# Performance work log

Hardware: AMD Instinct MI355X
Metric: run time of the kernel (lower is better)

## Reference

```python
import jax, jax.numpy as jnp
import numpy as np

B, T, F, D, HD = 16, 512, 16, 256, 256


def _init(k, shape, fan_in):
    return (jax.random.uniform(k, shape, minval=-1.0, maxval=1.0) / np.sqrt(fan_in)).astype(jnp.float32)


def setup_inputs() -> dict:
    key = jax.random.key(0)
    ks = jax.random.split(key, 16)
    return {
        "x": jax.random.normal(ks[0], (B, T, F), dtype=jnp.float32),
        # per-variable encoder params, batched over F (Linear(1,D) + GRN(D,HD,D))
        "w1": _init(ks[1], (F, D), 1), "b1": _init(ks[2], (F, D), 1),
        "fc1_w": _init(ks[3], (F, D, HD), D), "fc1_b": _init(ks[4], (F, HD), D),
        "fc2_w": _init(ks[5], (F, HD, D), HD), "fc2_b": _init(ks[6], (F, D), HD),
        "glu_w": _init(ks[7], (F, D, 2 * D), D), "glu_b": _init(ks[8], (F, 2 * D), D),
        "ln_g": jnp.ones((F, D), jnp.float32), "ln_b": jnp.zeros((F, D), jnp.float32),
        # weight GRN(F, HD, F); skip is Identity since d_in == d_out
        "wg_fc1_w": _init(ks[9], (F, HD), F), "wg_fc1_b": _init(ks[10], (HD,), F),
        "wg_fc2_w": _init(ks[11], (HD, F), HD), "wg_fc2_b": _init(ks[12], (F,), HD),
        "wg_glu_w": _init(ks[13], (F, 2 * F), F), "wg_glu_b": _init(ks[14], (2 * F,), F),
        "wg_ln_g": jnp.ones((F,), jnp.float32), "wg_ln_b": jnp.zeros((F,), jnp.float32),
    }


def _layernorm(x, g, b, eps=1e-5):
    m = jnp.mean(x, axis=-1, keepdims=True)
    v = jnp.var(x, axis=-1, keepdims=True)
    return (x - m) * jax.lax.rsqrt(v + eps) * g + b


def reference(x, w1, b1, fc1_w, fc1_b, fc2_w, fc2_b, glu_w, glu_b, ln_g, ln_b,
              wg_fc1_w, wg_fc1_b, wg_fc2_w, wg_fc2_b, wg_glu_w, wg_glu_b,
              wg_ln_g, wg_ln_b):
    # --- per-variable towers, batched over F (dropout is identity at eval) ---
    h0 = jax.nn.relu(x[..., None] * w1 + b1)                       # [B,T,F,D]
    y = jax.nn.elu(jnp.einsum('btfd,fdh->btfh', h0, fc1_w) + fc1_b)
    y = jnp.einsum('btfh,fhd->btfd', y, fc2_w) + fc2_b
    g = jnp.einsum('btfd,fde->btfe', y, glu_w) + glu_b             # [B,T,F,2D]
    a, gate = jnp.split(g, 2, axis=-1)
    H = _layernorm(h0 + a * jax.nn.sigmoid(gate), ln_g, ln_b)      # [B,T,F,D]
    # --- variable-weight GRN (time_distributed=True) ---
    yw = jax.nn.elu(x @ wg_fc1_w + wg_fc1_b)
    yw = yw @ wg_fc2_w + wg_fc2_b
    gw = x @ jnp.zeros((F, 0), x.dtype) if False else yw @ wg_glu_w + wg_glu_b
    aw, gatew = jnp.split(gw, 2, axis=-1)
    w = _layernorm(x + aw * jax.nn.sigmoid(gatew), wg_ln_g, wg_ln_b)
    w = jax.nn.softmax(w, axis=-1)                                 # [B,T,F]
    z = jnp.einsum('btfd,btf->btd', H, w)                          # [B,T,D]
    return z, w
```

## Files before the change

### kernel.cpp

```cpp
#include <hip/hip_runtime.h>
#include <hip/hip_bf16.h>

#define NBT 8192
#define NF  16
#define ND  256
#define NH  256
#define N2D 512

typedef short bf16x8 __attribute__((ext_vector_type(8)));
typedef float f32x4 __attribute__((ext_vector_type(4)));
typedef unsigned short u16x8 __attribute__((ext_vector_type(8)));

__device__ __forceinline__ float bf2f(unsigned short u) {
  return __uint_as_float(((unsigned)u) << 16);
}
__device__ __forceinline__ unsigned short f2bf(float f) {
  unsigned u = __float_as_uint(f);
  return (unsigned short)((u + 0x7FFFu + ((u >> 16) & 1u)) >> 16);
}

#define GLOAD16(src, dst)                                                     \
  __builtin_amdgcn_global_load_lds(                                           \
      (const __attribute__((address_space(1))) unsigned int*)(src),           \
      (__attribute__((address_space(3))) unsigned int*)(dst), 16, 0, 0)

__global__ __launch_bounds__(256) void wgrn_kernel(
    const float* __restrict__ x, const float* __restrict__ fw1,
    const float* __restrict__ fb1, const float* __restrict__ fw2,
    const float* __restrict__ fb2, const float* __restrict__ gwt,
    const float* __restrict__ gbt, const float* __restrict__ lng,
    const float* __restrict__ lnb, float* __restrict__ wout) {
  __shared__ float w1t[256 * 16];
  __shared__ float w2s[256 * 16];
  const int tid = threadIdx.x;
  for (int i = tid; i < 4096; i += 256) {
    int ff = i >> 8, j = i & 255;
    w1t[j * 16 + ff] = fw1[i];
    w2s[i] = fw2[i];
  }
  __syncthreads();
  const int sub  = tid & 7;
  const int rowi = tid >> 3;
  const int bt   = blockIdx.x * 32 + rowi;
  float xr[16];
#pragma unroll
  for (int i = 0; i < 4; ++i)
    *(float4*)&xr[i * 4] = *(const float4*)(x + (size_t)bt * 16 + i * 4);
  float acc2[16];
#pragma unroll
  for (int q = 0; q < 16; ++q) acc2[q] = 0.f;
  for (int j = sub; j < 256; j += 8) {
    float h = fb1[j];
    const float* wr = &w1t[j * 16];
#pragma unroll
    for (int q = 0; q < 16; ++q) h = fmaf(xr[q], wr[q], h);
    h = h > 0.f ? h : expm1f(h);
    const float* w2r = &w2s[j * 16];
#pragma unroll
    for (int q = 0; q < 16; ++q) acc2[q] = fmaf(h, w2r[q], acc2[q]);
  }
#pragma unroll
  for (int off = 1; off < 8; off <<= 1) {
#pragma unroll
    for (int q = 0; q < 16; ++q) acc2[q] += __shfl_xor(acc2[q], off);
  }
#pragma unroll
  for (int q = 0; q < 16; ++q) acc2[q] += fb2[q];
  float gw[32];
#pragma unroll
  for (int k = 0; k < 32; ++k) {
    float s = gbt[k];
#pragma unroll
    for (int q = 0; q < 16; ++q) s = fmaf(acc2[q], gwt[q * 32 + k], s);
    gw[k] = s;
  }
  float v[16];
  float mean = 0.f;
#pragma unroll
  for (int q = 0; q < 16; ++q) {
    float sg = 1.f / (1.f + __expf(-gw[16 + q]));
    v[q] = fmaf(gw[q], sg, xr[q]);
    mean += v[q];
  }
  mean *= (1.f / 16.f);
  float var = 0.f;
#pragma unroll
  for (int q = 0; q < 16; ++q) { float d = v[q] - mean; var = fmaf(d, d, var); }
  var *= (1.f / 16.f);
  float rstd = rsqrtf(var + 1e-5f);
  float mx = -1e30f;
#pragma unroll
  for (int q = 0; q < 16; ++q) {
    v[q] = (v[q] - mean) * rstd * lng[q] + lnb[q];
    mx = fmaxf(mx, v[q]);
  }
  float se = 0.f;
#pragma unroll
  for (int q = 0; q < 16; ++q) { v[q] = __expf(v[q] - mx); se += v[q]; }
  float inv = 1.f / se;
  if (sub == 0) {
#pragma unroll
    for (int i = 0; i < 4; ++i) {
      float4 o = { v[i*4+0]*inv, v[i*4+1]*inv, v[i*4+2]*inv, v[i*4+3]*inv };
      *(float4*)(wout + (size_t)bt * 16 + i * 4) = o;
    }
  }
}

__global__ void transpose_all(const float* __restrict__ fc1_w,
                              const float* __restrict__ fc2_w,
                              const float* __restrict__ glu_w,
                              unsigned short* __restrict__ fc1t,
                              unsigned short* __restrict__ fc2t,
                              unsigned short* __restrict__ glut) {
  __shared__ float tile[32][33];
  const int which = blockIdx.z >> 4;
  const int f     = blockIdx.z & 15;
  const float* src;
  unsigned short* dst;
  int K, N, bx = blockIdx.x;
  if (which == 0)      { src = fc1_w; dst = fc1t; K = ND; N = NH; }
  else if (which == 1) { src = fc2_w; dst = fc2t; K = NH; N = ND; }
  else                 { src = glu_w; dst = glut; K = ND; N = N2D;
                         bx += (which == 3) ? 8 : 0; }
  if (bx * 32 >= N) return;
  const float* s = src + (size_t)f * K * N;
  unsigned short* d = dst + (size_t)f * K * N;
  const int k0 = blockIdx.y * 32, n0 = bx * 32;
  const int tx = threadIdx.x, ty = threadIdx.y;
#pragma unroll
  for (int i = 0; i < 32; i += 8)
    tile[ty + i][tx] = s[(size_t)(k0 + ty + i) * N + n0 + tx];
  __syncthreads();
#pragma unroll
  for (int i = 0; i < 32; i += 8)
    d[(size_t)(n0 + ty + i) * K + k0 + tx] = f2bf(tile[tx][ty + i]);
}

__global__ __launch_bounds__(512, 2) void g12_kernel(
    const float* __restrict__ x, const float* __restrict__ w1,
    const float* __restrict__ b1, const unsigned short* __restrict__ fc1t,
    const float* __restrict__ fc1_b, const unsigned short* __restrict__ fc2t,
    const float* __restrict__ fc2_b, unsigned short* __restrict__ y2) {
  __shared__ __align__(16) unsigned short hbuf[64 * 264];
  __shared__ __align__(16) unsigned short bstg[256 * 64];
  __shared__ float xw[64];
  const int tid = threadIdx.x, lane = tid & 63, wid = tid >> 6;
  const int rl = lane & 15, kc = lane >> 4;
  int hb = blockIdx.x + 128 * blockIdx.y;
  int L  = (hb & 7) * 256 + (hb >> 3);
  const int f = L >> 7, m0 = (L & 127) * 64;
  const unsigned short* B1 = fc1t + (size_t)f * NH * ND;
  const unsigned short* B2 = fc2t + (size_t)f * ND * NH;
  const float* w1f = w1 + f * ND;
  const float* b1f = b1 + f * ND;
  const int wn = wid * 32;

  if (tid < 64) xw[tid] = x[(size_t)(m0 + tid) * NF + f];
  __syncthreads();

#pragma unroll
  for (int i = 0; i < 4; ++i) {
    int j = tid + 512 * i;
    int row = j >> 5, c = (j & 31) * 8;
    float xv = xw[row];
    float4 wa = *(const float4*)(w1f + c);
    float4 wb = *(const float4*)(w1f + c + 4);
    float4 ba = *(const float4*)(b1f + c);
    float4 bb = *(const float4*)(b1f + c + 4);
    u16x8 o;
    o[0] = f2bf(fmaxf(fmaf(xv, wa.x, ba.x), 0.f));
    o[1] = f2bf(fmaxf(fmaf(xv, wa.y, ba.y), 0.f));
    o[2] = f2bf(fmaxf(fmaf(xv, wa.z, ba.z), 0.f));
    o[3] = f2bf(fmaxf(fmaf(xv, wa.w, ba.w), 0.f));
    o[4] = f2bf(fmaxf(fmaf(xv, wb.x, bb.x), 0.f));
    o[5] = f2bf(fmaxf(fmaf(xv, wb.y, bb.y), 0.f));
    o[6] = f2bf(fmaxf(fmaf(xv, wb.z, bb.z), 0.f));
    o[7] = f2bf(fmaxf(fmaf(xv, wb.w, bb.w), 0.f));
    *(u16x8*)(hbuf + row * 264 + c) = o;
  }
  __syncthreads();

  f32x4 acc[4][2];
#pragma unroll
  for (int m = 0; m < 4; ++m)
#pragma unroll
    for (int n = 0; n < 2; ++n) acc[m][n] = (f32x4){0.f, 0.f, 0.f, 0.f};

  for (int kt = 0; kt < ND; kt += 64) {
    if (kt) __syncthreads();
#pragma unroll
    for (int i = 0; i < 4; ++i) {
      int s = tid + 512 * i;
      int row = s >> 3, sl = s & 7;
      GLOAD16(B1 + (size_t)row * ND + kt + ((sl ^ (row & 7)) << 3),
              (char*)bstg + (wid * 64 + 512 * i) * 16);
    }
    __syncthreads();
#pragma unroll
    for (int kk = 0; kk < 2; ++kk) {
      int s = kk * 4 + kc;
      bf16x8 av[4], bv[2];
#pragma unroll
      for (int n = 0; n < 2; ++n) {
        int rr = wn + n * 16 + rl;
        int ps = s ^ (rr & 7);
        bv[n] = *(const bf16x8*)((const char*)bstg + rr * 128 + ps * 16);
      }
#pragma unroll
      for (int m = 0; m < 4; ++m)
        av[m] = *(const bf16x8*)(hbuf + (m * 16 + rl) * 264 + kt + s * 8);
#pragma unroll
      for (int m = 0; m < 4; ++m)
#pragma unroll
        for (int n = 0; n < 2; ++n)
          acc[m][n] = __builtin_amdgcn_mfma_f32_16x16x32_bf16(av[m], bv[n],
                                                              acc[m][n], 0, 0, 0);
    }
  }
  __syncthreads();

#pragma unroll
  for (int n = 0; n < 2; ++n) {
    int c = wn + n * 16 + rl;
    float bvv = fc1_b[f * NH + c];
#pragma unroll
    for (int m = 0; m < 4; ++m) {
#pragma unroll
      for (int j = 0; j < 4; ++j) {
        int r = m * 16 + kc * 4 + j;
        float v = acc[m][n][j] + bvv;
        v = v > 0.f ? v : expm1f(v);
        hbuf[r * 264 + c] = f2bf(v);
      }
    }
  }
  __syncthreads();

#pragma unroll
  for (int m = 0; m < 4; ++m)
#pragma unroll
    for (int n = 0; n < 2; ++n) acc[m][n] = (f32x4){0.f, 0.f, 0.f, 0.f};

  for (int kt = 0; kt < NH; kt += 64) {
    if (kt) __syncthreads();
#pragma unroll
    for (int i = 0; i < 4; ++i) {
      int s = tid + 512 * i;
      int row = s >> 3, sl = s & 7;
      GLOAD16(B2 + (size_t)row * NH + kt + ((sl ^ (row & 7)) << 3),
              (char*)bstg + (wid * 64 + 512 * i) * 16);
    }
    __syncthreads();
#pragma unroll
    for (int kk = 0; kk < 2; ++kk) {
      int s = kk * 4 + kc;
      bf16x8 av[4], bv[2];
#pragma unroll
      for (int n = 0; n < 2; ++n) {
        int rr = wn + n * 16 + rl;
        int ps = s ^ (rr & 7);
        bv[n] = *(const bf16x8*)((const char*)bstg + rr * 128 + ps * 16);
      }
#pragma unroll
      for (int m = 0; m < 4; ++m)
        av[m] = *(const bf16x8*)(hbuf + (m * 16 + rl) * 264 + kt + s * 8);
#pragma unroll
      for (int m = 0; m < 4; ++m)
#pragma unroll
        for (int n = 0; n < 2; ++n)
          acc[m][n] = __builtin_amdgcn_mfma_f32_16x16x32_bf16(av[m], bv[n],
                                                              acc[m][n], 0, 0, 0);
    }
  }
  __syncthreads();

#pragma unroll
  for (int n = 0; n < 2; ++n) {
    int c = wn + n * 16 + rl;
    float bvv = fc2_b[f * ND + c];
#pragma unroll
    for (int m = 0; m < 4; ++m) {
#pragma unroll
      for (int j = 0; j < 4; ++j) {
        int r = m * 16 + kc * 4 + j;
        hbuf[r * 264 + c] = f2bf(acc[m][n][j] + bvv);
      }
    }
  }
  __syncthreads();
#pragma unroll
  for (int v = 0; v < 4; ++v) {
    int job = tid + 512 * v;
    int row = job >> 5, ch = job & 31;
    u16x8 val = *(const u16x8*)(hbuf + row * 264 + ch * 8);
    *(u16x8*)(y2 + ((size_t)f * NBT + m0 + row) * ND + ch * 8) = val;
  }
}

__global__ __launch_bounds__(512, 4) void g3_kernel(
    const unsigned short* __restrict__ y2,
    const unsigned short* __restrict__ glut, const float* __restrict__ glu_b,
    const float* __restrict__ x, const float* __restrict__ w1,
    const float* __restrict__ b1, const float* __restrict__ ln_g,
    const float* __restrict__ ln_b, unsigned short* __restrict__ H) {
  __shared__ __align__(16) char arena[73728];
  __shared__ float xw[64];
  __shared__ float2 sums[8][64];
  __shared__ float2 sums2[64];
  unsigned short* abuf = (unsigned short*)arena;
  unsigned short* bbuf = (unsigned short*)(arena + 8192);
  unsigned short* vbuf = (unsigned short*)arena;

  const int tid = threadIdx.x, lane = tid & 63, wid = tid >> 6;
  const int rl = lane & 15, rq = lane >> 4;
  int hb = blockIdx.x + 128 * blockIdx.y;
  int L  = (hb & 7) * 256 + (hb >> 3);
  const int f = L >> 7, m0 = (L & 127) * 64;
  const unsigned short* Af = y2 + (size_t)f * NBT * ND;
  const unsigned short* Bf = glut + (size_t)f * ND * N2D;
  const float* w1f = w1 + f * ND;
  const float* b1f = b1 + f * ND;
  const int colb = wid * 32;
  if (tid < 64) xw[tid] = x[(size_t)(m0 + tid) * NF + f];

  f32x4 acc[4][4];
#pragma unroll
  for (int m = 0; m < 4; ++m)
#pragma unroll
    for (int n = 0; n < 4; ++n) acc[m][n] = (f32x4){0.f, 0.f, 0.f, 0.f};

  for (int kt = 0; kt < ND; kt += 64) {
    __syncthreads();
    {
      int s = tid;
      int row = s >> 3, sl = s & 7;
      const unsigned short* ga =
          Af + (size_t)(m0 + row) * ND + kt + ((sl ^ (row & 7)) << 3);
      GLOAD16(ga, (char*)abuf + (wid * 64) * 16);
    }
#pragma unroll
    for (int i = 0; i < 8; ++i) {
      int s = tid + 512 * i;
      int row = s >> 3, sl = s & 7;
      const unsigned short* gb =
          Bf + (size_t)row * ND + kt + ((sl ^ (row & 7)) << 3);
      GLOAD16(gb, (char*)bbuf + (wid * 64 + 512 * i) * 16);
    }
    __syncthreads();
#pragma unroll
    for (int kk = 0; kk < 2; ++kk) {
      bf16x8 av[4], bv[4];
      int s = kk * 4 + rq;
#pragma unroll
      for (int m = 0; m < 4; ++m) {
        int r = m * 16 + rl;
        int ps = s ^ (r & 7);
        av[m] = *(const bf16x8*)((const char*)abuf + r * 128 + ps * 16);
      }
#pragma unroll
      for (int n = 0; n < 4; ++n) {
        int rr = (n < 2) ? (colb + n * 16 + rl)
                         : (256 + colb + (n - 2) * 16 + rl);
        int ps = s ^ (rr & 7);
        bv[n] = *(const bf16x8*)((const char*)bbuf + rr * 128 + ps * 16);
      }
#pragma unroll
      for (int m = 0; m < 4; ++m)
#pragma unroll
        for (int n = 0; n < 4; ++n)
          acc[m][n] = __builtin_amdgcn_mfma_f32_16x16x32_bf16(av[m], bv[n],
                                                              acc[m][n], 0, 0, 0);
    }
  }

#pragma unroll
  for (int n = 0; n < 2; ++n) {
    int cA = colb + n * 16 + rl;
    float ab_ = glu_b[f * N2D + cA];
    float gb_ = glu_b[f * N2D + 256 + cA];
    float w1c = w1f[cA], b1c = b1f[cA];
#pragma unroll
    for (int m = 0; m < 4; ++m) {
#pragma unroll
      for (int j = 0; j < 4; ++j) {
        int r = m * 16 + rq * 4 + j;
        float a = acc[m][n][j] + ab_;
        float g = acc[m][n + 2][j] + gb_;
        float sg = 1.f / (1.f + __expf(-g));
        float h0 = fmaxf(fmaf(xw[r], w1c, b1c), 0.f);
        acc[m][n][j] = fmaf(a, sg, h0);
      }
    }
  }
#pragma unroll
  for (int m = 0; m < 4; ++m) {
#pragma unroll
    for (int j = 0; j < 4; ++j) {
      float s = acc[m][0][j] + acc[m][1][j];
      float q = fmaf(acc[m][0][j], acc[m][0][j],
                     acc[m][1][j] * acc[m][1][j]);
#pragma unroll
      for (int off = 1; off < 16; off <<= 1) {
        s += __shfl_xor(s, off);
        q += __shfl_xor(q, off);
      }
      if (rl == 0) sums[wid][m * 16 + rq * 4 + j] = make_float2(s, q);
    }
  }
  __syncthreads();
  if (tid < 64) {
    float tot = 0.f, tot2 = 0.f;
#pragma unroll
    for (int wv = 0; wv < 8; ++wv) {
      float2 p = sums[wv][tid];
      tot += p.x;
      tot2 += p.y;
    }
    float mean = tot * (1.f / 256.f);
    float var  = tot2 * (1.f / 256.f) - mean * mean;
    sums2[tid] = make_float2(mean, rsqrtf(var + 1e-5f));
  }
  __syncthreads();
#pragma unroll
  for (int n = 0; n < 2; ++n) {
    int cA = colb + n * 16 + rl;
    float lg = ln_g[f * ND + cA], lb = ln_b[f * ND + cA];
#pragma unroll
    for (int m = 0; m < 4; ++m) {
#pragma unroll
      for (int j = 0; j < 4; ++j) {
        int r = m * 16 + rq * 4 + j;
        float2 mr = sums2[r];
        vbuf[r * 264 + cA] = f2bf(fmaf((acc[m][n][j] - mr.x) * mr.y, lg, lb));
      }
    }
  }
  __syncthreads();
  {
    int row = tid >> 3, chunk = tid & 7;
    unsigned short* Hrow = H + ((size_t)f * NBT + m0 + row) * ND;
#pragma unroll
    for (int v = 0; v < 4; ++v) {
      u16x8 val = *(const u16x8*)(vbuf + row * 264 + chunk * 8 + v * 64);
      *(u16x8*)(Hrow + chunk * 8 + v * 64) = val;
    }
  }
}

__global__ __launch_bounds__(256) void combine_kernel(
    const unsigned short* __restrict__ H, const float* __restrict__ w,
    float* __restrict__ z) {
  int idx = blockIdx.x * 256 + threadIdx.x;
  int bt = idx >> 5;
  int d  = (idx & 31) << 3;
  float a[8];
#pragma unroll
  for (int j = 0; j < 8; ++j) a[j] = 0.f;
#pragma unroll
  for (int f = 0; f < 16; ++f) {
    u16x8 hv = *(const u16x8*)(H + ((size_t)f * NBT + bt) * ND + d);
    float wvv = w[bt * 16 + f];
#pragma unroll
    for (int j = 0; j < 8; ++j) a[j] = fmaf(bf2f(hv[j]), wvv, a[j]);
  }
  float4 o0 = {a[0], a[1], a[2], a[3]};
  float4 o1 = {a[4], a[5], a[6], a[7]};
  *(float4*)(z + (size_t)bt * ND + d)     = o0;
  *(float4*)(z + (size_t)bt * ND + d + 4) = o1;
}

extern "C" void kernel_launch(void* const* d_in, const int* in_sizes, int n_in,
                              void* d_out, int out_size, void* d_ws,
                              size_t ws_size, hipStream_t stream) {
  const float* x        = (const float*)d_in[0];
  const float* w1       = (const float*)d_in[1];
  const float* b1       = (const float*)d_in[2];
  const float* fc1_w    = (const float*)d_in[3];
  const float* fc1_b    = (const float*)d_in[4];
  const float* fc2_w    = (const float*)d_in[5];
  const float* fc2_b    = (const float*)d_in[6];
  const float* glu_w    = (const float*)d_in[7];
  const float* glu_b    = (const float*)d_in[8];
  const float* ln_g     = (const float*)d_in[9];
  const float* ln_b     = (const float*)d_in[10];
  const float* wg_fc1_w = (const float*)d_in[11];
  const float* wg_fc1_b = (const float*)d_in[12];
  const float* wg_fc2_w = (const float*)d_in[13];
  const float* wg_fc2_b = (const float*)d_in[14];
  const float* wg_glu_w = (const float*)d_in[15];
  const float* wg_glu_b = (const float*)d_in[16];
  const float* wg_ln_g  = (const float*)d_in[17];
  const float* wg_ln_b  = (const float*)d_in[18];

  char* ws = (char*)d_ws;
  unsigned short* fc1t = (unsigned short*)ws;
  unsigned short* fc2t = fc1t + (size_t)NF * NH * ND;
  unsigned short* glut = fc2t + (size_t)NF * ND * NH;
  unsigned short* y2   = (unsigned short*)(ws + (8ull << 20));
  unsigned short* Hbuf = (unsigned short*)(ws + (72ull << 20));

  float* zout = (float*)d_out;
  float* wout = zout + (size_t)NBT * ND;

  wgrn_kernel<<<256, 256, 0, stream>>>(x, wg_fc1_w, wg_fc1_b, wg_fc2_w,
                                       wg_fc2_b, wg_glu_w, wg_glu_b, wg_ln_g,
                                       wg_ln_b, wout);
  transpose_all<<<dim3(16, 8, 64), dim3(32, 8), 0, stream>>>(
      fc1_w, fc2_w, glu_w, fc1t, fc2t, glut);

  g12_kernel<<<dim3(128, 16), 512, 0, stream>>>(x, w1, b1, fc1t, fc1_b, fc2t,
                                                fc2_b, y2);
  g3_kernel<<<dim3(128, 16), 512, 0, stream>>>(y2, glut, glu_b, x, w1, b1,
                                               ln_g, ln_b, Hbuf);
  combine_kernel<<<(NBT * ND / 8) / 256, 256, 0, stream>>>(Hbuf, wout, zout);

  (void)in_sizes; (void)n_in; (void)out_size; (void)ws_size;
}
```

Measured before the change: 195.5 us.

## Fuse GLU GEMM and layernorm into tower kernel, dropping y2 round-trip

Folds the third GEMM (GLU), its gating and the layernorm into the fc1/fc2 kernel, so the fc2 output stays in LDS (hbuf) instead of being written to and re-read from global memory as y2. One kernel launch and a 64MB intermediate round-trip go away. In exchange, the fused kernel stages GLU weights through the existing bstg buffer in 32-wide k-slices with a sync per slice. It runs at the g12 occupancy (2 blocks/CU) rather than g3's 4, and holds an extra 16-tile accumulator set, which adds register pressure.

```diff
diff --git a/kernel.cpp b/kernel.cpp
--- a/kernel.cpp
+++ b/kernel.cpp
@@ -137,14 +137,19 @@
     d[(size_t)(n0 + ty + i) * K + k0 + tx] = f2bf(tile[tx][ty + i]);
 }
 
-__global__ __launch_bounds__(512, 2) void g12_kernel(
+__global__ __launch_bounds__(512, 2) void tower_kernel(
     const float* __restrict__ x, const float* __restrict__ w1,
-    const float* __restrict__ b1, const unsigned short* __restrict__ fc1t,
-    const float* __restrict__ fc1_b, const unsigned short* __restrict__ fc2t,
-    const float* __restrict__ fc2_b, unsigned short* __restrict__ y2) {
+    const float* __restrict__ b1,
+    const unsigned short* __restrict__ fc1t, const float* __restrict__ fc1_b,
+    const unsigned short* __restrict__ fc2t, const float* __restrict__ fc2_b,
+    const unsigned short* __restrict__ glut, const float* __restrict__ glu_b,
+    const float* __restrict__ ln_g, const float* __restrict__ ln_b,
+    unsigned short* __restrict__ H) {
   __shared__ __align__(16) unsigned short hbuf[64 * 264];
   __shared__ __align__(16) unsigned short bstg[256 * 64];
   __shared__ float xw[64];
+  __shared__ float2 sums[8][64];
+  __shared__ float2 sums2[64];
   const int tid = threadIdx.x, lane = tid & 63, wid = tid >> 6;
   const int rl = lane & 15, kc = lane >> 4;
   int hb = blockIdx.x + 128 * blockIdx.y;
@@ -152,6 +157,7 @@
   const int f = L >> 7, m0 = (L & 127) * 64;
   const unsigned short* B1 = fc1t + (size_t)f * NH * ND;
   const unsigned short* B2 = fc2t + (size_t)f * ND * NH;
+  const unsigned short* B3 = glut + (size_t)f * ND * N2D;
   const float* w1f = w1 + f * ND;
   const float* b1f = b1 + f * ND;
   const int wn = wid * 32;
@@ -289,162 +295,111 @@
     }
   }
   __syncthreads();
+
+  f32x4 acc3[4][4];
+#pragma unroll
+  for (int m = 0; m < 4; ++m)
+#pragma unroll
+    for (int n = 0; n < 4; ++n) acc3[m][n] = (f32x4){0.f, 0.f, 0.f, 0.f};
+
+  for (int t = 0; t < 8; ++t) {
+    if (t) __syncthreads();
+#pragma unroll
+    for (int i = 0; i < 4; ++i) {
+      int g = tid + 512 * i;
+      int row = g >> 2, sl = g & 3;
+      int srcg = sl ^ ((row >> 1) & 3);
+      GLOAD16(B3 + (size_t)row * ND + t * 32 + srcg * 8,
+              (char*)bstg + (size_t)g * 16);
+    }
+    __syncthreads();
+    bf16x8 av[4], bv[4];
+#pragma unroll
+    for (int m = 0; m < 4; ++m)
+      av[m] = *(const bf16x8*)(hbuf + (m * 16 + rl) * 264 + t * 32 + kc * 8);
+#pragma unroll
+    for (int n = 0; n < 4; ++n) {
+      int brow = (n < 2) ? (wn + n * 16 + rl) : (256 + wn + (n - 2) * 16 + rl);
+      int g = kc ^ ((brow >> 1) & 3);
+      bv[n] = *(const bf16x8*)((const char*)bstg + brow * 64 + g * 16);
+    }
+#pragma unroll
+    for (int m = 0; m < 4; ++m)
+#pragma unroll
+      for (int n = 0; n < 4; ++n)
+        acc3[m][n] = __builtin_amdgcn_mfma_f32_16x16x32_bf16(av[m], bv[n],
+                                                             acc3[m][n], 0, 0, 0);
+  }
+
+#pragma unroll
+  for (int n = 0; n < 2; ++n) {
+    int cA = wn + n * 16 + rl;
+    float ab_ = glu_b[f * N2D + cA];
+    float gb_ = glu_b[f * N2D + 256 + cA];
+    float w1c = w1f[cA], b1c = b1f[cA];
+#pragma unroll
+    for (int m = 0; m < 4; ++m) {
+#pragma unroll
+      for (int j = 0; j < 4; ++j) {
+        int r = m * 16 + kc * 4 + j;
+        float a = acc3[m][n][j] + ab_;
+        float g = acc3[m][n + 2][j] + gb_;
+        float sg = 1.f / (1.f + __expf(-g));
+        float h0 = fmaxf(fmaf(xw[r], w1c, b1c), 0.f);
+        acc3[m][n][j] = fmaf(a, sg, h0);
+      }
+    }
+  }
+#pragma unroll
+  for (int m = 0; m < 4; ++m) {
+#pragma unroll
+    for (int j = 0; j < 4; ++j) {
+      float s = acc3[m][0][j] + acc3[m][1][j];
+      float q = fmaf(acc3[m][0][j], acc3[m][0][j],
+                     acc3[m][1][j] * acc3[m][1][j]);
+#pragma unroll
+      for (int off = 1; off < 16; off <<= 1) {
+        s += __shfl_xor(s, off);
+        q += __shfl_xor(q, off);
+      }
+      if (rl == 0) sums[wid][m * 16 + kc * 4 + j] = make_float2(s, q);
+    }
+  }
+  __syncthreads();
+  if (tid < 64) {
+    float tot = 0.f, tot2 = 0.f;
+#pragma unroll
+    for (int wv = 0; wv < 8; ++wv) {
+      float2 p = sums[wv][tid];
+      tot += p.x;
+      tot2 += p.y;
+    }
+    float mean = tot * (1.f / 256.f);
+    float var  = tot2 * (1.f / 256.f) - mean * mean;
+    sums2[tid] = make_float2(mean, rsqrtf(var + 1e-5f));
+  }
+  __syncthreads();
+#pragma unroll
+  for (int n = 0; n < 2; ++n) {
+    int cA = wn + n * 16 + rl;
+    float lg = ln_g[f * ND + cA], lb = ln_b[f * ND + cA];
+#pragma unroll
+    for (int m = 0; m < 4; ++m) {
+#pragma unroll
+      for (int j = 0; j < 4; ++j) {
+        int r = m * 16 + kc * 4 + j;
+        float2 mr = sums2[r];
+        hbuf[r * 264 + cA] = f2bf(fmaf((acc3[m][n][j] - mr.x) * mr.y, lg, lb));
+      }
+    }
+  }
+  __syncthreads();
 #pragma unroll
   for (int v = 0; v < 4; ++v) {
     int job = tid + 512 * v;
     int row = job >> 5, ch = job & 31;
     u16x8 val = *(const u16x8*)(hbuf + row * 264 + ch * 8);
-    *(u16x8*)(y2 + ((size_t)f * NBT + m0 + row) * ND + ch * 8) = val;
-  }
-}
-
-__global__ __launch_bounds__(512, 4) void g3_kernel(
-    const unsigned short* __restrict__ y2,
-    const unsigned short* __restrict__ glut, const float* __restrict__ glu_b,
-    const float* __restrict__ x, const float* __restrict__ w1,
-    const float* __restrict__ b1, const float* __restrict__ ln_g,
-    const float* __restrict__ ln_b, unsigned short* __restrict__ H) {
-  __shared__ __align__(16) char arena[73728];
-  __shared__ float xw[64];
-  __shared__ float2 sums[8][64];
-  __shared__ float2 sums2[64];
-  unsigned short* abuf = (unsigned short*)arena;
-  unsigned short* bbuf = (unsigned short*)(arena + 8192);
-  unsigned short* vbuf = (unsigned short*)arena;
-
-  const int tid = threadIdx.x, lane = tid & 63, wid = tid >> 6;
-  const int rl = lane & 15, rq = lane >> 4;
-  int hb = blockIdx.x + 128 * blockIdx.y;
-  int L  = (hb & 7) * 256 + (hb >> 3);
-  const int f = L >> 7, m0 = (L & 127) * 64;
-  const unsigned short* Af = y2 + (size_t)f * NBT * ND;
-  const unsigned short* Bf = glut + (size_t)f * ND * N2D;
-  const float* w1f = w1 + f * ND;
-  const float* b1f = b1 + f * ND;
-  const int colb = wid * 32;
-  if (tid < 64) xw[tid] = x[(size_t)(m0 + tid) * NF + f];
-
-  f32x4 acc[4][4];
-#pragma unroll
-  for (int m = 0; m < 4; ++m)
-#pragma unroll
-    for (int n = 0; n < 4; ++n) acc[m][n] = (f32x4){0.f, 0.f, 0.f, 0.f};
-
-  for (int kt = 0; kt < ND; kt += 64) {
-    __syncthreads();
-    {
-      int s = tid;
-      int row = s >> 3, sl = s & 7;
-      const unsigned short* ga =
-          Af + (size_t)(m0 + row) * ND + kt + ((sl ^ (row & 7)) << 3);
-      GLOAD16(ga, (char*)abuf + (wid * 64) * 16);
-    }
-#pragma unroll
-    for (int i = 0; i < 8; ++i) {
-      int s = tid + 512 * i;
-      int row = s >> 3, sl = s & 7;
-      const unsigned short* gb =
-          Bf + (size_t)row * ND + kt + ((sl ^ (row & 7)) << 3);
-      GLOAD16(gb, (char*)bbuf + (wid * 64 + 512 * i) * 16);
-    }
-    __syncthreads();
-#pragma unroll
-    for (int kk = 0; kk < 2; ++kk) {
-      bf16x8 av[4], bv[4];
-      int s = kk * 4 + rq;
-#pragma unroll
-      for (int m = 0; m < 4; ++m) {
-        int r = m * 16 + rl;
-        int ps = s ^ (r & 7);
-        av[m] = *(const bf16x8*)((const char*)abuf + r * 128 + ps * 16);
-      }
-#pragma unroll
-      for (int n = 0; n < 4; ++n) {
-        int rr = (n < 2) ? (colb + n * 16 + rl)
-                         : (256 + colb + (n - 2) * 16 + rl);
-        int ps = s ^ (rr & 7);
-        bv[n] = *(const bf16x8*)((const char*)bbuf + rr * 128 + ps * 16);
-      }
-#pragma unroll
-      for (int m = 0; m < 4; ++m)
-#pragma unroll
-        for (int n = 0; n < 4; ++n)
-          acc[m][n] = __builtin_amdgcn_mfma_f32_16x16x32_bf16(av[m], bv[n],
-                                                              acc[m][n], 0, 0, 0);
-    }
-  }
-
-#pragma unroll
-  for (int n = 0; n < 2; ++n) {
-    int cA = colb + n * 16 + rl;
-    float ab_ = glu_b[f * N2D + cA];
-    float gb_ = glu_b[f * N2D + 256 + cA];
-    float w1c = w1f[cA], b1c = b1f[cA];
-#pragma unroll
-    for (int m = 0; m < 4; ++m) {
-#pragma unroll
-      for (int j = 0; j < 4; ++j) {
-        int r = m * 16 + rq * 4 + j;
-        float a = acc[m][n][j] + ab_;
-        float g = acc[m][n + 2][j] + gb_;
-        float sg = 1.f / (1.f + __expf(-g));
-        float h0 = fmaxf(fmaf(xw[r], w1c, b1c), 0.f);
-        acc[m][n][j] = fmaf(a, sg, h0);
-      }
-    }
-  }
-#pragma unroll
-  for (int m = 0; m < 4; ++m) {
-#pragma unroll
-    for (int j = 0; j < 4; ++j) {
-      float s = acc[m][0][j] + acc[m][1][j];
-      float q = fmaf(acc[m][0][j], acc[m][0][j],
-                     acc[m][1][j] * acc[m][1][j]);
-#pragma unroll
-      for (int off = 1; off < 16; off <<= 1) {
-        s += __shfl_xor(s, off);
-        q += __shfl_xor(q, off);
-      }
-      if (rl == 0) sums[wid][m * 16 + rq * 4 + j] = make_float2(s, q);
-    }
-  }
-  __syncthreads();
-  if (tid < 64) {
-    float tot = 0.f, tot2 = 0.f;
-#pragma unroll
-    for (int wv = 0; wv < 8; ++wv) {
-      float2 p = sums[wv][tid];
-      tot += p.x;
-      tot2 += p.y;
-    }
-    float mean = tot * (1.f / 256.f);
-    float var  = tot2 * (1.f / 256.f) - mean * mean;
-    sums2[tid] = make_float2(mean, rsqrtf(var + 1e-5f));
-  }
-  __syncthreads();
-#pragma unroll
-  for (int n = 0; n < 2; ++n) {
-    int cA = colb + n * 16 + rl;
-    float lg = ln_g[f * ND + cA], lb = ln_b[f * ND + cA];
-#pragma unroll
-    for (int m = 0; m < 4; ++m) {
-#pragma unroll
-      for (int j = 0; j < 4; ++j) {
-        int r = m * 16 + rq * 4 + j;
-        float2 mr = sums2[r];
-        vbuf[r * 264 + cA] = f2bf(fmaf((acc[m][n][j] - mr.x) * mr.y, lg, lb));
-      }
-    }
-  }
-  __syncthreads();
-  {
-    int row = tid >> 3, chunk = tid & 7;
-    unsigned short* Hrow = H + ((size_t)f * NBT + m0 + row) * ND;
-#pragma unroll
-    for (int v = 0; v < 4; ++v) {
-      u16x8 val = *(const u16x8*)(vbuf + row * 264 + chunk * 8 + v * 64);
-      *(u16x8*)(Hrow + chunk * 8 + v * 64) = val;
-    }
+    *(u16x8*)(H + ((size_t)f * NBT + m0 + row) * ND + ch * 8) = val;
   }
 }
 
@@ -497,8 +452,7 @@
   unsigned short* fc1t = (unsigned short*)ws;
   unsigned short* fc2t = fc1t + (size_t)NF * NH * ND;
   unsigned short* glut = fc2t + (size_t)NF * ND * NH;
-  unsigned short* y2   = (unsigned short*)(ws + (8ull << 20));
-  unsigned short* Hbuf = (unsigned short*)(ws + (72ull << 20));
+  unsigned short* Hbuf = (unsigned short*)(ws + (8ull << 20));
 
   float* zout = (float*)d_out;
   float* wout = zout + (size_t)NBT * ND;
@@ -509,10 +463,9 @@
   transpose_all<<<dim3(16, 8, 64), dim3(32, 8), 0, stream>>>(
       fc1_w, fc2_w, glu_w, fc1t, fc2t, glut);
 
-  g12_kernel<<<dim3(128, 16), 512, 0, stream>>>(x, w1, b1, fc1t, fc1_b, fc2t,
-                                                fc2_b, y2);
-  g3_kernel<<<dim3(128, 16), 512, 0, stream>>>(y2, glut, glu_b, x, w1, b1,
-                                               ln_g, ln_b, Hbuf);
+  tower_kernel<<<dim3(128, 16), 512, 0, stream>>>(
+      x, w1, b1, fc1t, fc1_b, fc2t, fc2_b, glut, glu_b, ln_g, ln_b, Hbuf);
+
   combine_kernel<<<(NBT * ND / 8) / 256, 256, 0, stream>>>(Hbuf, wout, zout);
 
   (void)in_sizes; (void)n_in; (void)out_size; (void)ws_size;
```

New measurement: 235.5 us. 20.4% more time.
